# Optimization experiments

Measured on AMD Instinct MI355X. Metric: run time of the kernel, lower is better.

Reference implementation:

```python
import jax, jax.numpy as jnp
import numpy as np

B, D, Q = 256, 2048, 880880
NUM_CLASSES = 1000
T_K = 10.0  # self.T_k


def setup_inputs() -> dict:
    key = jax.random.key(0)
    k1, k2, k3, k4, k5, k6 = jax.random.split(key, 6)
    return {
        "features": jax.random.normal(k1, (B, D), dtype=jnp.float32),
        "labels": jax.random.randint(k2, (B,), 0, NUM_CLASSES),
        "pred": jax.random.randint(k3, (B,), 0, NUM_CLASSES),
        "confidence": jax.random.uniform(k4, (B,), dtype=jnp.float32),
        "queue_mus": jax.random.normal(k5, (Q,), dtype=jnp.float32),
        "queue_sigmas": jax.random.uniform(k6, (Q,), dtype=jnp.float32),
    }


def reference(features, labels, pred, confidence, queue_mus, queue_sigmas):
    # Per-sample feature statistics (torch.std is unbiased -> ddof=1)
    means = jnp.mean(features, axis=1)              # [B]
    stds = jnp.std(features, axis=1, ddof=1)        # [B]
    # Broadcast pairwise 'Wasserstein' distance vs queue: [B, Q]
    wd = jnp.sqrt((means[:, None] - queue_mus[None, :]) ** 2
                  + (stds[:, None] - queue_sigmas[None, :]) ** 2)
    min_distances = jnp.min(wd, axis=1)             # [B]
    # T_scale == 0 branch: T = exp(-T_k * min_dist)
    T = jnp.exp(-T_K * min_distances)
    return T
```

## Files before the change

### kernel.cpp

```cpp
#include <hip/hip_runtime.h>
#include <math.h>

#define NB 256
#define ND 2048
#define T_K 10.0f
#define LDSCAP 2048

__global__ __launch_bounds__(256) void stats_kernel(const float* __restrict__ feat,
                                                    float* __restrict__ stats) {
    const int b   = blockIdx.x;
    const int tid = threadIdx.x;
    const int lane = tid & 63, wid = tid >> 6;
    __shared__ float ls[4], lq[4];

    const float4* row = (const float4*)(feat + (size_t)b * ND);
    float sum = 0.f, sumsq = 0.f;
#pragma unroll
    for (int i = 0; i < 2; ++i) {
        float4 v = row[tid + i * 256];
        sum   += v.x + v.y + v.z + v.w;
        sumsq += v.x * v.x + v.y * v.y + v.z * v.z + v.w * v.w;
    }
#pragma unroll
    for (int off = 32; off > 0; off >>= 1) {
        sum   += __shfl_down(sum, off, 64);
        sumsq += __shfl_down(sumsq, off, 64);
    }
    if (lane == 0) { ls[wid] = sum; lq[wid] = sumsq; }
    __syncthreads();
    if (tid == 0) {
        float S  = ls[0] + ls[1] + ls[2] + ls[3];
        float Q2 = lq[0] + lq[1] + lq[2] + lq[3];
        float mean = S / (float)ND;
        float var  = fmaxf((Q2 - S * mean) / (float)(ND - 1), 0.f);
        stats[b]      = mean;
        stats[NB + b] = sqrtf(var);
    }
}

__global__ __launch_bounds__(256) void scan_pruned_kernel(const float* __restrict__ mus,
                                                          const float* __restrict__ sigmas,
                                                          const float* __restrict__ stats,
                                                          float* __restrict__ partial,
                                                          int Q) {
    const int b    = blockIdx.x;
    const int tid  = threadIdx.x;
    const int lane = tid & 63, wid = tid >> 6;

    __shared__ float2 buf[LDSCAP];
    __shared__ float  red[4][NB];
    __shared__ float  ls[4], lq[4];
    __shared__ int    cnt;

    const int nquad = Q >> 2;
    const int chunk = (nquad + NB - 1) / NB;
    const int qs    = b * chunk;
    const int qe    = min(qs + chunk, nquad);
    const float4* mu4 = (const float4*)mus;
    const float4* sg4 = (const float4*)sigmas;

    float best = INFINITY;
    for (int i = qs + tid; i < qe; i += 256) {
        float4 mu = mu4[i], sg = sg4[i];
        float s0 = sg.x - 1.f, s1 = sg.y - 1.f, s2e = sg.z - 1.f, s3 = sg.w - 1.f;
        best = fminf(best, fmaf(mu.x, mu.x, s0 * s0));
        best = fminf(best, fmaf(mu.y, mu.y, s1 * s1));
        best = fminf(best, fmaf(mu.z, mu.z, s2e * s2e));
        best = fminf(best, fmaf(mu.w, mu.w, s3 * s3));
    }
    if (b == 0) {
        int q = nquad * 4 + tid;
        if (q < Q) {
            float dm = mus[q], ds = sigmas[q] - 1.f;
            best = fminf(best, fmaf(dm, dm, ds * ds));
        }
    }

    const float mb = stats[tid], sb = stats[NB + tid];
    {
        float dsb = sb - 1.f;
        float r2 = fmaf(mb, mb, dsb * dsb);
#pragma unroll
        for (int off = 32; off > 0; off >>= 1) {
            best = fminf(best, __shfl_down(best, off, 64));
            r2   = fmaxf(r2,   __shfl_down(r2,   off, 64));
        }
        if (lane == 0) { ls[wid] = best; lq[wid] = r2; }
        if (tid == 0) cnt = 0;
    }
    __syncthreads();
    const float U0   = fminf(fminf(ls[0], ls[1]), fminf(ls[2], ls[3]));
    const float R2   = fmaxf(fmaxf(lq[0], lq[1]), fmaxf(lq[2], lq[3]));
    const float thr  = sqrtf(U0) + 2.f * sqrtf(R2);
    const float thr2 = thr * thr * 1.0001f + 1e-12f;

    float m2[4], s2[4];
#pragma unroll
    for (int k = 0; k < 4; ++k) {
        m2[k] = -2.f * stats[lane + 64 * k];
        s2[k] = -2.f * stats[NB + lane + 64 * k];
    }
    float acc[4];
#pragma unroll
    for (int k = 0; k < 4; ++k) acc[k] = INFINITY;

    for (int base = qs; base < qe; base += 256) {
        __syncthreads();
        if (cnt > LDSCAP - 1024) {
            const int n = cnt;
            for (int j = wid; j < n; j += 4) {
                float2 p = buf[j];
                float r = fmaf(p.x, p.x, p.y * p.y);
#pragma unroll
                for (int k = 0; k < 4; ++k)
                    acc[k] = fminf(acc[k], fmaf(m2[k], p.x, fmaf(s2[k], p.y, r)));
            }
            __syncthreads();
            if (tid == 0) cnt = 0;
            __syncthreads();
        }
        const int i = base + tid;
        if (i < qe) {
            float4 mu = mu4[i], sg = sg4[i];
#define TESTK(MX, SX)                                                        \
            {                                                                \
                float dm = (MX), dss = (SX) - 1.f;                           \
                float dd = fmaf(dm, dm, dss * dss);                          \
                if (dd <= thr2) {                                            \
                    int p = atomicAdd(&cnt, 1);                              \
                    buf[p] = make_float2((MX), (SX));                        \
                }                                                            \
            }
            TESTK(mu.x, sg.x)
            TESTK(mu.y, sg.y)
            TESTK(mu.z, sg.z)
            TESTK(mu.w, sg.w)
        }
    }
    if (b == 0) {
        int q = nquad * 4 + tid;
        if (q < Q) { TESTK(mus[q], sigmas[q]) }
    }
#undef TESTK

    __syncthreads();
    {
        const int n = cnt;
        for (int j = wid; j < n; j += 4) {
            float2 p = buf[j];
            float r = fmaf(p.x, p.x, p.y * p.y);
#pragma unroll
            for (int k = 0; k < 4; ++k)
                acc[k] = fminf(acc[k], fmaf(m2[k], p.x, fmaf(s2[k], p.y, r)));
        }
    }

    __syncthreads();
#pragma unroll
    for (int k = 0; k < 4; ++k) red[wid][lane + 64 * k] = acc[k];
    __syncthreads();
    {
        float v = fminf(fminf(red[0][tid], red[1][tid]), fminf(red[2][tid], red[3][tid]));
        v = v + fmaf(mb, mb, sb * sb);
        partial[(size_t)b * NB + tid] = fmaxf(v, 0.f);
    }
}

__global__ __launch_bounds__(256) void reduce_kernel(const float* __restrict__ partial,
                                                     float* __restrict__ out) {
    const int b   = blockIdx.x;
    const int tid = threadIdx.x;
    const int lane = tid & 63, wid = tid >> 6;
    float v = partial[(size_t)tid * NB + b];
#pragma unroll
    for (int off = 32; off > 0; off >>= 1)
        v = fminf(v, __shfl_down(v, off, 64));
    __shared__ float w[4];
    if (lane == 0) w[wid] = v;
    __syncthreads();
    if (tid == 0) {
        float m = fminf(fminf(w[0], w[1]), fminf(w[2], w[3]));
        out[b] = expf(-T_K * sqrtf(m));
    }
}

extern "C" void kernel_launch(void* const* d_in, const int* in_sizes, int n_in,
                              void* d_out, int out_size, void* d_ws, size_t ws_size,
                              hipStream_t stream) {
    const float* features = (const float*)d_in[0];
    const float* queue_mus    = (const float*)d_in[4];
    const float* queue_sigmas = (const float*)d_in[5];
    const int Q = in_sizes[4];

    float* stats   = (float*)d_ws;
    float* partial = stats + 2 * NB;

    stats_kernel<<<NB, 256, 0, stream>>>(features, stats);
    scan_pruned_kernel<<<NB, 256, 0, stream>>>(queue_mus, queue_sigmas, stats,
                                               partial, Q);
    reduce_kernel<<<NB, 256, 0, stream>>>(partial, (float*)d_out);
}
```

Measured before the change: 19.09 us.

## Restructure pruned scan into global filter list with wider probe grid

Fuses the feature-stats computation with the per-chunk probe pass over a 1024-block grid. A separate filter kernel uses a global pruning threshold and appends surviving queue entries to a global list through an atomic counter. A final kernel has each batch row scan that compacted list directly. The aim is to expose more parallelism over the queue and to drop the per-block 256-row candidate evaluation and the partial-reduce pass. In exchange it adds global atomics and a second full read of the queue, and the final per-row scan cost grows with the number of survivors.

```diff
diff --git a/kernel.cpp b/kernel.cpp
--- a/kernel.cpp
+++ b/kernel.cpp
@@ -4,58 +4,53 @@
 #define NB 256
 #define ND 2048
 #define T_K 10.0f
-#define LDSCAP 2048
-
-__global__ __launch_bounds__(256) void stats_kernel(const float* __restrict__ feat,
-                                                    float* __restrict__ stats) {
-    const int b   = blockIdx.x;
-    const int tid = threadIdx.x;
+#define PGRID 1024
+#define FCAP 1024
+
+__global__ __launch_bounds__(256) void stats_probe_kernel(const float* __restrict__ feat,
+                                                          const float* __restrict__ mus,
+                                                          const float* __restrict__ sigmas,
+                                                          float* __restrict__ stats,
+                                                          float* __restrict__ u0part,
+                                                          unsigned int* __restrict__ gcount,
+                                                          int Q) {
+    const int b = blockIdx.x, tid = threadIdx.x;
     const int lane = tid & 63, wid = tid >> 6;
     __shared__ float ls[4], lq[4];
 
-    const float4* row = (const float4*)(feat + (size_t)b * ND);
-    float sum = 0.f, sumsq = 0.f;
-#pragma unroll
-    for (int i = 0; i < 2; ++i) {
-        float4 v = row[tid + i * 256];
-        sum   += v.x + v.y + v.z + v.w;
-        sumsq += v.x * v.x + v.y * v.y + v.z * v.z + v.w * v.w;
-    }
-#pragma unroll
-    for (int off = 32; off > 0; off >>= 1) {
-        sum   += __shfl_down(sum, off, 64);
-        sumsq += __shfl_down(sumsq, off, 64);
-    }
-    if (lane == 0) { ls[wid] = sum; lq[wid] = sumsq; }
-    __syncthreads();
-    if (tid == 0) {
-        float S  = ls[0] + ls[1] + ls[2] + ls[3];
-        float Q2 = lq[0] + lq[1] + lq[2] + lq[3];
-        float mean = S / (float)ND;
-        float var  = fmaxf((Q2 - S * mean) / (float)(ND - 1), 0.f);
-        stats[b]      = mean;
-        stats[NB + b] = sqrtf(var);
-    }
-}
-
-__global__ __launch_bounds__(256) void scan_pruned_kernel(const float* __restrict__ mus,
-                                                          const float* __restrict__ sigmas,
-                                                          const float* __restrict__ stats,
-                                                          float* __restrict__ partial,
-                                                          int Q) {
-    const int b    = blockIdx.x;
-    const int tid  = threadIdx.x;
-    const int lane = tid & 63, wid = tid >> 6;
-
-    __shared__ float2 buf[LDSCAP];
-    __shared__ float  red[4][NB];
-    __shared__ float  ls[4], lq[4];
-    __shared__ int    cnt;
+    if (b == 0 && tid == 0) gcount[0] = 0u;
+
+    if (b < NB) {
+        const float4* row = (const float4*)(feat + (size_t)b * ND);
+        float sum = 0.f, sumsq = 0.f;
+#pragma unroll
+        for (int i = 0; i < 2; ++i) {
+            float4 v = row[tid + i * 256];
+            sum   += v.x + v.y + v.z + v.w;
+            sumsq += v.x * v.x + v.y * v.y + v.z * v.z + v.w * v.w;
+        }
+#pragma unroll
+        for (int off = 32; off > 0; off >>= 1) {
+            sum   += __shfl_down(sum, off, 64);
+            sumsq += __shfl_down(sumsq, off, 64);
+        }
+        if (lane == 0) { ls[wid] = sum; lq[wid] = sumsq; }
+        __syncthreads();
+        if (tid == 0) {
+            float S  = ls[0] + ls[1] + ls[2] + ls[3];
+            float Q2 = lq[0] + lq[1] + lq[2] + lq[3];
+            float mean = S / (float)ND;
+            float var  = fmaxf((Q2 - S * mean) / (float)(ND - 1), 0.f);
+            stats[b]      = mean;
+            stats[NB + b] = sqrtf(var);
+        }
+        __syncthreads();
+    }
 
     const int nquad = Q >> 2;
-    const int chunk = (nquad + NB - 1) / NB;
-    const int qs    = b * chunk;
-    const int qe    = min(qs + chunk, nquad);
+    const int spq   = (nquad + PGRID - 1) / PGRID;
+    const int qs    = b * spq;
+    const int qe    = min(qs + spq, nquad);
     const float4* mu4 = (const float4*)mus;
     const float4* sg4 = (const float4*)sigmas;
 
@@ -75,17 +70,43 @@
             best = fminf(best, fmaf(dm, dm, ds * ds));
         }
     }
-
-    const float mb = stats[tid], sb = stats[NB + tid];
+#pragma unroll
+    for (int off = 32; off > 0; off >>= 1)
+        best = fminf(best, __shfl_down(best, off, 64));
+    if (lane == 0) ls[wid] = best;
+    __syncthreads();
+    if (tid == 0)
+        u0part[b] = fminf(fminf(ls[0], ls[1]), fminf(ls[2], ls[3]));
+}
+
+__global__ __launch_bounds__(256) void filter_kernel(const float* __restrict__ mus,
+                                                     const float* __restrict__ sigmas,
+                                                     const float* __restrict__ stats,
+                                                     const float* __restrict__ u0part,
+                                                     unsigned int* __restrict__ gcount,
+                                                     float2* __restrict__ glist,
+                                                     int Q) {
+    const int b = blockIdx.x, tid = threadIdx.x;
+    const int lane = tid & 63, wid = tid >> 6;
+
+    __shared__ float2 buf[FCAP];
+    __shared__ float  ls[4], lq[4];
+    __shared__ int    cnt;
+    __shared__ unsigned int gbase;
+
     {
-        float dsb = sb - 1.f;
+        float u = INFINITY;
+#pragma unroll
+        for (int j = 0; j < PGRID / 256; ++j)
+            u = fminf(u, u0part[tid + j * 256]);
+        float mb = stats[tid], dsb = stats[NB + tid] - 1.f;
         float r2 = fmaf(mb, mb, dsb * dsb);
 #pragma unroll
         for (int off = 32; off > 0; off >>= 1) {
-            best = fminf(best, __shfl_down(best, off, 64));
-            r2   = fmaxf(r2,   __shfl_down(r2,   off, 64));
-        }
-        if (lane == 0) { ls[wid] = best; lq[wid] = r2; }
+            u  = fminf(u,  __shfl_down(u,  off, 64));
+            r2 = fmaxf(r2, __shfl_down(r2, off, 64));
+        }
+        if (lane == 0) { ls[wid] = u; lq[wid] = r2; }
         if (tid == 0) cnt = 0;
     }
     __syncthreads();
@@ -94,27 +115,20 @@
     const float thr  = sqrtf(U0) + 2.f * sqrtf(R2);
     const float thr2 = thr * thr * 1.0001f + 1e-12f;
 
-    float m2[4], s2[4];
-#pragma unroll
-    for (int k = 0; k < 4; ++k) {
-        m2[k] = -2.f * stats[lane + 64 * k];
-        s2[k] = -2.f * stats[NB + lane + 64 * k];
-    }
-    float acc[4];
-#pragma unroll
-    for (int k = 0; k < 4; ++k) acc[k] = INFINITY;
+    const int nquad = Q >> 2;
+    const int spq   = (nquad + PGRID - 1) / PGRID;
+    const int qs    = b * spq;
+    const int qe    = min(qs + spq, nquad);
+    const float4* mu4 = (const float4*)mus;
+    const float4* sg4 = (const float4*)sigmas;
 
     for (int base = qs; base < qe; base += 256) {
         __syncthreads();
-        if (cnt > LDSCAP - 1024) {
+        if (cnt > FCAP - 1024) {
             const int n = cnt;
-            for (int j = wid; j < n; j += 4) {
-                float2 p = buf[j];
-                float r = fmaf(p.x, p.x, p.y * p.y);
-#pragma unroll
-                for (int k = 0; k < 4; ++k)
-                    acc[k] = fminf(acc[k], fmaf(m2[k], p.x, fmaf(s2[k], p.y, r)));
-            }
+            if (tid == 0) gbase = atomicAdd(gcount, (unsigned int)n);
+            __syncthreads();
+            for (int j = tid; j < n; j += 256) glist[gbase + j] = buf[j];
             __syncthreads();
             if (tid == 0) cnt = 0;
             __syncthreads();
@@ -146,41 +160,37 @@
     __syncthreads();
     {
         const int n = cnt;
-        for (int j = wid; j < n; j += 4) {
-            float2 p = buf[j];
-            float r = fmaf(p.x, p.x, p.y * p.y);
-#pragma unroll
-            for (int k = 0; k < 4; ++k)
-                acc[k] = fminf(acc[k], fmaf(m2[k], p.x, fmaf(s2[k], p.y, r)));
-        }
-    }
-
-    __syncthreads();
-#pragma unroll
-    for (int k = 0; k < 4; ++k) red[wid][lane + 64 * k] = acc[k];
-    __syncthreads();
-    {
-        float v = fminf(fminf(red[0][tid], red[1][tid]), fminf(red[2][tid], red[3][tid]));
-        v = v + fmaf(mb, mb, sb * sb);
-        partial[(size_t)b * NB + tid] = fmaxf(v, 0.f);
-    }
-}
-
-__global__ __launch_bounds__(256) void reduce_kernel(const float* __restrict__ partial,
-                                                     float* __restrict__ out) {
-    const int b   = blockIdx.x;
-    const int tid = threadIdx.x;
+        if (tid == 0) gbase = atomicAdd(gcount, (unsigned int)n);
+        __syncthreads();
+        for (int j = tid; j < n; j += 256) glist[gbase + j] = buf[j];
+    }
+}
+
+__global__ __launch_bounds__(256) void gather_scan_kernel(const float2* __restrict__ glist,
+                                                          const unsigned int* __restrict__ gcount,
+                                                          const float* __restrict__ stats,
+                                                          float* __restrict__ out) {
+    const int b = blockIdx.x, tid = threadIdx.x;
     const int lane = tid & 63, wid = tid >> 6;
-    float v = partial[(size_t)tid * NB + b];
+    __shared__ float w[4];
+
+    const float mb = stats[b], sb = stats[NB + b];
+    const int n = (int)gcount[0];
+
+    float best = INFINITY;
+    for (int j = tid; j < n; j += 256) {
+        float2 p = glist[j];
+        float dm = mb - p.x, ds = sb - p.y;
+        best = fminf(best, fmaf(dm, dm, ds * ds));
+    }
 #pragma unroll
     for (int off = 32; off > 0; off >>= 1)
-        v = fminf(v, __shfl_down(v, off, 64));
-    __shared__ float w[4];
-    if (lane == 0) w[wid] = v;
+        best = fminf(best, __shfl_down(best, off, 64));
+    if (lane == 0) w[wid] = best;
     __syncthreads();
     if (tid == 0) {
         float m = fminf(fminf(w[0], w[1]), fminf(w[2], w[3]));
-        out[b] = expf(-T_K * sqrtf(m));
+        out[b] = expf(-T_K * sqrtf(fmaxf(m, 0.f)));
     }
 }
 
@@ -192,11 +202,14 @@
     const float* queue_sigmas = (const float*)d_in[5];
     const int Q = in_sizes[4];
 
-    float* stats   = (float*)d_ws;
-    float* partial = stats + 2 * NB;
-
-    stats_kernel<<<NB, 256, 0, stream>>>(features, stats);
-    scan_pruned_kernel<<<NB, 256, 0, stream>>>(queue_mus, queue_sigmas, stats,
-                                               partial, Q);
-    reduce_kernel<<<NB, 256, 0, stream>>>(partial, (float*)d_out);
-}
+    float*        stats  = (float*)d_ws;
+    float*        u0part = stats + 2 * NB;
+    unsigned int* gcount = (unsigned int*)(u0part + PGRID);
+    float2*       glist  = (float2*)(gcount + 2);
+
+    stats_probe_kernel<<<PGRID, 256, 0, stream>>>(features, queue_mus, queue_sigmas,
+                                                  stats, u0part, gcount, Q);
+    filter_kernel<<<PGRID, 256, 0, stream>>>(queue_mus, queue_sigmas, stats, u0part,
+                                             gcount, glist, Q);
+    gather_scan_kernel<<<NB, 256, 0, stream>>>(glist, gcount, stats, (float*)d_out);
+}
```

Result: slower. 37.26 us (+95.1%).
